# Kernel optimization log

Measured on AMD Instinct MI355X. Metric: run time of the kernel, lower is better.

Reference implementation:

```python
import jax, jax.numpy as jnp
import numpy as np

# Model hyperparameters (from init_kwargs)
B, C, H, W = 4, 3, 224, 224
P = 16            # patch size
E = 768           # embed_dim
NH = 12           # num_heads
DH = E // NH      # head dim
L = 2             # num_layers
DFF = 4 * E
OUT = 1000
NP_ = (H // P) * (W // P)   # 196 patches
ALPHA, BETA, GAMMA = 0.5, 0.5, 1.0
EPS = 1e-8
LN_EPS = 1e-5


def _layernorm(x, w, b):
    mu = x.mean(-1, keepdims=True)
    var = ((x - mu) ** 2).mean(-1, keepdims=True)
    return (x - mu) * jax.lax.rsqrt(var + LN_EPS) * w + b


def _tversky_attn(x, ln_w, ln_b, w_qkv, b_qkv, w_o, b_o):
    # x: [B,S,E]
    h = _layernorm(x, ln_w, ln_b)
    qkv = h @ w_qkv + b_qkv                       # [B,S,3E]
    q, k, v = jnp.split(qkv, 3, axis=-1)
    def heads(t):
        return t.reshape(t.shape[0], t.shape[1], NH, DH).transpose(0, 2, 1, 3)  # [B,NH,S,DH]
    q, k, v = heads(q), heads(k), heads(v)
    # Tversky similarity on non-negative feature memberships
    qp = jax.nn.relu(q)
    kp = jax.nn.relu(k)
    qs = qp.sum(-1)                               # [B,NH,S]
    ks = kp.sum(-1)                               # [B,NH,S]
    # pairwise L1: sum_d |q_i - k_j|   (dominant intermediate [B,NH,S,S,DH])
    l1 = jnp.abs(qp[:, :, :, None, :] - kp[:, :, None, :, :]).sum(-1)  # [B,NH,S,S]
    qsum = qs[:, :, :, None]
    ksum = ks[:, :, None, :]
    inter = 0.5 * (qsum + ksum - l1)              # sum min(q,k)
    a_minus_b = 0.5 * (l1 + qsum - ksum)          # sum relu(q-k)
    b_minus_a = 0.5 * (l1 - qsum + ksum)          # sum relu(k-q)
    scores = GAMMA * inter / (inter + ALPHA * a_minus_b + BETA * b_minus_a + EPS)
    attn = jax.nn.softmax(scores, axis=-1)        # [B,NH,S,S]
    o = jnp.einsum('bhij,bhjd->bhid', attn, v)    # [B,NH,S,DH]
    o = o.transpose(0, 2, 1, 3).reshape(x.shape[0], x.shape[1], E)
    return o @ w_o + b_o


def _forward(x, conv_w, conv_b, pos_embed, cls_token,
             ln1_w, ln1_b, attn_w, attn_b, proj_w, proj_b,
             ln2_w, ln2_b, fc1_w, fc1_b, fc2_w, fc2_b,
             lnf_w, lnf_b, head_w, head_b):
    b = x.shape[0]
    # patch embed: stride==kernel conv == non-overlapping patch projection
    xp = x.reshape(b, C, H // P, P, W // P, P)
    tok = jnp.einsum('bchpwq,ecpq->bhwe', xp, conv_w).reshape(b, NP_, E) + conv_b
    tok = tok + pos_embed                         # [B,196,E]
    cls = jnp.broadcast_to(cls_token, (b, 1, E))
    h = jnp.concatenate([cls, tok], axis=1)       # [B,197,E]
    for i in range(L):
        h = h + _tversky_attn(h, ln1_w[i], ln1_b[i], attn_w[i], attn_b[i], proj_w[i], proj_b[i])
        m = _layernorm(h, ln2_w[i], ln2_b[i])
        m = jax.nn.gelu(m @ fc1_w[i] + fc1_b[i])
        h = h + m @ fc2_w[i] + fc2_b[i]
    h = _layernorm(h, lnf_w, lnf_b)
    return h[:, 0] @ head_w + head_b              # [B,OUT]


def setup_inputs() -> dict:
    key = jax.random.key(0)
    ks = jax.random.split(key, 24)
    n = lambda k, shp, s=0.02: jax.random.normal(k, shp, dtype=jnp.float32) * s
    return {
        'x': jax.random.normal(ks[0], (B, C, H, W), dtype=jnp.float32),
        'conv_w': n(ks[1], (E, C, P, P)),
        'conv_b': jnp.zeros((E,), jnp.float32),
        'pos_embed': n(ks[2], (1, NP_, E)),
        'cls_token': n(ks[3], (1, 1, E)),
        'ln1_w': jnp.ones((L, E), jnp.float32),
        'ln1_b': jnp.zeros((L, E), jnp.float32),
        'attn_w': n(ks[4], (L, E, 3 * E)),
        'attn_b': jnp.zeros((L, 3 * E), jnp.float32),
        'proj_w': n(ks[5], (L, E, E)),
        'proj_b': jnp.zeros((L, E), jnp.float32),
        'ln2_w': jnp.ones((L, E), jnp.float32),
        'ln2_b': jnp.zeros((L, E), jnp.float32),
        'fc1_w': n(ks[6], (L, E, DFF)),
        'fc1_b': jnp.zeros((L, DFF), jnp.float32),
        'fc2_w': n(ks[7], (L, DFF, E)),
        'fc2_b': jnp.zeros((L, E), jnp.float32),
        'lnf_w': jnp.ones((E,), jnp.float32),
        'lnf_b': jnp.zeros((E,), jnp.float32),
        'head_w': n(ks[8], (E, OUT)),
        'head_b': jnp.zeros((OUT,), jnp.float32),
    }


def reference(x, conv_w, conv_b, pos_embed, cls_token,
              ln1_w, ln1_b, attn_w, attn_b, proj_w, proj_b,
              ln2_w, ln2_b, fc1_w, fc1_b, fc2_w, fc2_b,
              lnf_w, lnf_b, head_w, head_b):
    return _forward(x, conv_w, conv_b, pos_embed, cls_token,
                    ln1_w, ln1_b, attn_w, attn_b, proj_w, proj_b,
                    ln2_w, ln2_b, fc1_w, fc1_b, fc2_w, fc2_b,
                    lnf_w, lnf_b, head_w, head_b)
```

## Files before the change

### kernel.cpp

```cpp
#include <hip/hip_runtime.h>
#include <hip/hip_bf16.h>
#include <math.h>

#define B_  4
#define E_  768
#define NH_ 12
#define DH_ 64
#define DFF_ 3072
#define OUT_ 1000
#define S_  197
#define ROWS_ 788
#define QH_P 12608
#define KGP  16384

typedef __bf16 bf16x8_t __attribute__((ext_vector_type(8)));
typedef float f32x4_t __attribute__((ext_vector_type(4)));
typedef _Float16 f16x2_t __attribute__((ext_vector_type(2)));

#define HAS_FDOT2 __has_builtin(__builtin_amdgcn_fdot2)

__device__ __forceinline__ float gelu_f(float x) {
    float x3 = x * x * x;
    return 0.5f * x * (1.0f + tanhf(0.7978845608028654f * (x + 0.044715f * x3)));
}
__device__ __forceinline__ ushort f_to_bf16bits(float f) {
    __hip_bfloat16 b = __float2bfloat16(f);
    return *(ushort*)&b;
}
__device__ __forceinline__ ushort f_to_f16bits(float f) {
    _Float16 h = (_Float16)f;
    return __builtin_bit_cast(ushort, h);
}
__device__ __forceinline__ f16x2_t u2h(uint u) { return __builtin_bit_cast(f16x2_t, u); }
__device__ __forceinline__ f16x2_t min2(f16x2_t a, f16x2_t b) {
    return __builtin_elementwise_min(a, b);
}

#define WT_CONV   0
#define WT_LBASE  589824
#define WT_LSTRIDE 7077888
#define WT_QKV    0
#define WT_PROJ   1769472
#define WT_FC1    2359296
#define WT_FC2    4718592
__global__ __launch_bounds__(256) void prep_all_kernel(const float* __restrict__ x,
                                                       __hip_bfloat16* __restrict__ aim,
                                                       const float* __restrict__ attn_w,
                                                       const float* __restrict__ proj_w,
                                                       const float* __restrict__ fc1_w,
                                                       const float* __restrict__ fc2_w,
                                                       const float* __restrict__ conv_w,
                                                       __hip_bfloat16* __restrict__ wt,
                                                       ushort* __restrict__ vgt) {
    int bid = blockIdx.x;
    if (bid < 588) {
        int id = bid * 256 + threadIdx.x;
        int row = id / 192, k4 = (id - row * 192) * 4;
        int b = row / 196, pr = row - b * 196;
        int hp = pr / 14, wp = pr - hp * 14;
        int c = k4 >> 8, rem = k4 & 255, p = rem >> 4, q = rem & 15;
        float4 v = *(const float4*)&x[(((size_t)(b * 3 + c) * 224) + hp * 16 + p) * 224 + wp * 16 + q];
        ushort4 o = make_ushort4(f_to_bf16bits(v.x), f_to_bf16bits(v.y), f_to_bf16bits(v.z), f_to_bf16bits(v.w));
        *(ushort4*)((ushort*)aim + (size_t)row * 768 + k4) = o;
        return;
    }
    int id = bid - 588;
    if (id < 3456) {
        int l = id / 1728, r = id - l * 1728;
        const float* src;
        __hip_bfloat16* dst;
        int K, N, tile;
        size_t lbase = WT_LBASE + (size_t)l * WT_LSTRIDE;
        if (r < 432)       { src = attn_w + (size_t)l * E_ * 3 * E_; dst = wt + lbase + WT_QKV;  K = E_;   N = 3 * E_; tile = r; }
        else if (r < 576)  { src = proj_w + (size_t)l * E_ * E_;     dst = wt + lbase + WT_PROJ; K = E_;   N = E_;     tile = r - 432; }
        else if (r < 1152) { src = fc1_w + (size_t)l * E_ * DFF_;    dst = wt + lbase + WT_FC1;  K = E_;   N = DFF_;   tile = r - 576; }
        else               { src = fc2_w + (size_t)l * DFF_ * E_;    dst = wt + lbase + WT_FC2;  K = DFF_; N = E_;     tile = r - 1152; }
        int ntn = N >> 6;
        int kb = (tile / ntn) * 64, nb = (tile % ntn) * 64;
        int kq = (threadIdx.x & 15) * 4, nq = (threadIdx.x >> 4) * 4;
        const float* s0 = src + (size_t)(kb + kq) * N + nb + nq;
        float4 v0 = *(const float4*)(s0);
        float4 v1 = *(const float4*)(s0 + N);
        float4 v2 = *(const float4*)(s0 + 2 * N);
        float4 v3 = *(const float4*)(s0 + 3 * N);
        __hip_bfloat16* d0 = dst + (size_t)(nb + nq) * K + kb + kq;
        *(ushort4*)(d0)         = make_ushort4(f_to_bf16bits(v0.x), f_to_bf16bits(v1.x), f_to_bf16bits(v2.x), f_to_bf16bits(v3.x));
        *(ushort4*)(d0 + K)     = make_ushort4(f_to_bf16bits(v0.y), f_to_bf16bits(v1.y), f_to_bf16bits(v2.y), f_to_bf16bits(v3.y));
        *(ushort4*)(d0 + 2 * K) = make_ushort4(f_to_bf16bits(v0.z), f_to_bf16bits(v1.z), f_to_bf16bits(v2.z), f_to_bf16bits(v3.z));
        *(ushort4*)(d0 + 3 * K) = make_ushort4(f_to_bf16bits(v0.w), f_to_bf16bits(v1.w), f_to_bf16bits(v2.w), f_to_bf16bits(v3.w));
        return;
    }
    id -= 3456;
    if (id < 576) {
        int off = (id * 256 + threadIdx.x) * 4;
        float4 v = *(const float4*)&conv_w[off];
        ushort4 o = make_ushort4(f_to_bf16bits(v.x), f_to_bf16bits(v.y), f_to_bf16bits(v.z), f_to_bf16bits(v.w));
        *(ushort4*)((ushort*)wt + WT_CONV + off) = o;
        return;
    }
    id -= 576;
    {
        int off = (id * 256 + threadIdx.x) * 4;
        *(ushort4*)&vgt[off] = make_ushort4(0, 0, 0, 0);
    }
}

#define BK 64
#define AP 72
__global__ __launch_bounds__(256) void gemm_mfma_kernel(const __hip_bfloat16* __restrict__ A,
                                                        const __hip_bfloat16* __restrict__ WT,
                                                        const float* __restrict__ bias,
                                                        const float* __restrict__ res,
                                                        float* __restrict__ Cf,
                                                        __hip_bfloat16* __restrict__ Cb,
                                                        float* __restrict__ partbase,
                                                        int M, int N, int K, int act, int KS,
                                                        int res_pitch, int pn, int nofs) {
    __shared__ __align__(16) ushort Asb[2][64 * AP];
    __shared__ __align__(16) ushort Bsb[2][64 * AP];
    const int tid = threadIdx.x;
    const int wave = tid >> 6, lane = tid & 63;
    const int quad = lane >> 4, l15 = lane & 15;
    const int wm = wave >> 1, wn = wave & 1;
    const int m0 = blockIdx.y * 64, n0 = blockIdx.x * 64;

    const int Kc   = K / KS;
    const int kbeg = blockIdx.z * Kc;
    const int n_it = Kc / BK;

    f32x4_t acc[2][2] = {};

    const int c0r = tid >> 3,         c0o = (tid & 7) * 8;
    const int c1r = (tid + 256) >> 3, c1o = c0o;

    uint4 pa0, pa1, pb0, pb1;
    auto load_tile = [&](int kk) {
        pa0 = make_uint4(0, 0, 0, 0);
        pa1 = pa0;
        int gm = m0 + c0r;
        if (gm < M) pa0 = *(const uint4*)&A[(size_t)gm * K + kk + c0o];
        gm = m0 + c1r;
        if (gm < M) pa1 = *(const uint4*)&A[(size_t)gm * K + kk + c1o];
        pb0 = *(const uint4*)&WT[(size_t)(n0 + c0r) * K + kk + c0o];
        pb1 = *(const uint4*)&WT[(size_t)(n0 + c1r) * K + kk + c1o];
    };
    auto store_tile = [&](int buf) {
        *(uint4*)&Asb[buf][c0r * AP + c0o] = pa0;
        *(uint4*)&Asb[buf][c1r * AP + c1o] = pa1;
        *(uint4*)&Bsb[buf][c0r * AP + c0o] = pb0;
        *(uint4*)&Bsb[buf][c1r * AP + c1o] = pb1;
    };

    load_tile(kbeg);
    store_tile(0);
    if (n_it > 1) load_tile(kbeg + BK);
    __syncthreads();

    for (int it = 0; it < n_it; ++it) {
        const int cur = it & 1, nxt = cur ^ 1;
        if (it + 1 < n_it) {
            store_tile(nxt);
            if (it + 2 < n_it) load_tile(kbeg + (it + 2) * BK);
        }
        const ushort* As = Asb[cur];
        const ushort* Bs = Bsb[cur];
#pragma unroll
        for (int ks = 0; ks < BK; ks += 32) {
            bf16x8_t a0 = *(const bf16x8_t*)&As[(32 * wm + l15) * AP + ks + 8 * quad];
            bf16x8_t a1 = *(const bf16x8_t*)&As[(32 * wm + 16 + l15) * AP + ks + 8 * quad];
            bf16x8_t b0 = *(const bf16x8_t*)&Bs[(32 * wn + l15) * AP + ks + 8 * quad];
            bf16x8_t b1 = *(const bf16x8_t*)&Bs[(32 * wn + 16 + l15) * AP + ks + 8 * quad];
            acc[0][0] = __builtin_amdgcn_mfma_f32_16x16x32_bf16(a0, b0, acc[0][0], 0, 0, 0);
            acc[0][1] = __builtin_amdgcn_mfma_f32_16x16x32_bf16(a0, b1, acc[0][1], 0, 0, 0);
            acc[1][0] = __builtin_amdgcn_mfma_f32_16x16x32_bf16(a1, b0, acc[1][0], 0, 0, 0);
            acc[1][1] = __builtin_amdgcn_mfma_f32_16x16x32_bf16(a1, b1, acc[1][1], 0, 0, 0);
        }
        __syncthreads();
    }

    if (partbase) {
        float* P = partbase + (size_t)blockIdx.z * M * pn;
#pragma unroll
        for (int mi = 0; mi < 2; ++mi)
#pragma unroll
            for (int ni = 0; ni < 2; ++ni) {
                int gn = n0 + 32 * wn + 16 * ni + l15;
#pragma unroll
                for (int r = 0; r < 4; ++r) {
                    int gm = m0 + 32 * wm + 16 * mi + quad * 4 + r;
                    if (gm < M) P[(size_t)gm * pn + nofs + gn] = acc[mi][ni][r];
                }
            }
        return;
    }

#pragma unroll
    for (int mi = 0; mi < 2; ++mi)
#pragma unroll
        for (int ni = 0; ni < 2; ++ni) {
            int gn = n0 + 32 * wn + 16 * ni + l15;
#pragma unroll
            for (int r = 0; r < 4; ++r) {
                int gm = m0 + 32 * wm + 16 * mi + quad * 4 + r;
                if (gm < M) {
                    float v = acc[mi][ni][r] + bias[gn];
                    if (act == 1) v = gelu_f(v);
                    if (res) v += res[(size_t)gm * res_pitch + gn];
                    if (Cf) Cf[(size_t)gm * N + gn] = v;
                    else    Cb[(size_t)gm * N + gn] = __float2bfloat16(v);
                }
            }
        }
}

__global__ __launch_bounds__(256) void gemm_qkv_kernel(const __hip_bfloat16* __restrict__ A,
                                                       const __hip_bfloat16* __restrict__ WT,
                                                       const float* __restrict__ ab,
                                                       ushort* __restrict__ qg,
                                                       float* __restrict__ qsg,
                                                       ushort* __restrict__ kg,
                                                       float* __restrict__ ksg,
                                                       ushort* __restrict__ vgt,
                                                       int ncol0, int nqkv,
                                                       const float* __restrict__ wraw) {
    const int tid = threadIdx.x;
    const int wave = tid >> 6, lane = tid & 63;

    if ((int)blockIdx.x >= nqkv) {
        if (blockIdx.y >= NH_) return;
        const int hh = blockIdx.y, bb = blockIdx.x - nqkv;
        const int head = bb * NH_ + hh;
        __shared__ float sacc[4][64];
        const __hip_bfloat16* xr = A + (size_t)(bb * S_) * E_;
        const float* wcol = wraw + hh * DH_;
        float acc = 0.f;
        const int k0 = wave * 192;
#pragma unroll 4
        for (int k = k0; k < k0 + 192; ++k)
            acc += __bfloat162float(xr[k]) * wcol[(size_t)k * (3 * E_) + lane];
        sacc[wave][lane] = acc;
        __syncthreads();
        if (tid < 64) {
            float q = sacc[0][tid] + sacc[1][tid] + sacc[2][tid] + sacc[3][tid] + ab[hh * DH_ + tid];
            q = fmaxf(q, 0.f);
            qg[(size_t)head * QH_P + tid] = f_to_f16bits(q);
            float s = q;
#pragma unroll
            for (int m = 1; m < 64; m <<= 1) s += __shfl_xor(s, m, 64);
            if (tid == 0) qsg[(size_t)head * 200] = s;
        }
        return;
    }

    __shared__ __align__(16) ushort Asb[2][64 * AP];
    __shared__ __align__(16) ushort Bsb[2][64 * AP];
    __shared__ float rs[2][64];
    const int quad = lane >> 4, l15 = lane & 15;
    const int wm = wave >> 1, wn = wave & 1;
    const int m0 = blockIdx.y * 64;
    const int n0g = ncol0 + blockIdx.x * 64;

    f32x4_t acc[2][2] = {};

    const int c0r = tid >> 3,         c0o = (tid & 7) * 8;
    const int c1r = (tid + 256) >> 3, c1o = c0o;

    uint4 pa0, pa1, pb0, pb1;
    auto load_tile = [&](int kk) {
        pa0 = make_uint4(0, 0, 0, 0);
        pa1 = pa0;
        int gm = m0 + c0r;
        if (gm < ROWS_) pa0 = *(const uint4*)&A[(size_t)gm * E_ + kk + c0o];
        gm = m0 + c1r;
        if (gm < ROWS_) pa1 = *(const uint4*)&A[(size_t)gm * E_ + kk + c1o];
        pb0 = *(const uint4*)&WT[(size_t)(n0g + c0r) * E_ + kk + c0o];
        pb1 = *(const uint4*)&WT[(size_t)(n0g + c1r) * E_ + kk + c1o];
    };
    auto store_tile = [&](int buf) {
        *(uint4*)&Asb[buf][c0r * AP + c0o] = pa0;
        *(uint4*)&Asb[buf][c1r * AP + c1o] = pa1;
        *(uint4*)&Bsb[buf][c0r * AP + c0o] = pb0;
        *(uint4*)&Bsb[buf][c1r * AP + c1o] = pb1;
    };

    load_tile(0);
    store_tile(0);
    load_tile(BK);
    __syncthreads();

    const int n_it = E_ / BK;
    for (int it = 0; it < n_it; ++it) {
        const int cur = it & 1, nxt = cur ^ 1;
        if (it + 1 < n_it) {
            store_tile(nxt);
            if (it + 2 < n_it) load_tile((it + 2) * BK);
        }
        const ushort* As = Asb[cur];
        const ushort* Bs = Bsb[cur];
#pragma unroll
        for (int ks = 0; ks < BK; ks += 32) {
            bf16x8_t a0 = *(const bf16x8_t*)&As[(32 * wm + l15) * AP + ks + 8 * quad];
            bf16x8_t a1 = *(const bf16x8_t*)&As[(32 * wm + 16 + l15) * AP + ks + 8 * quad];
            bf16x8_t b0 = *(const bf16x8_t*)&Bs[(32 * wn + l15) * AP + ks + 8 * quad];
            bf16x8_t b1 = *(const bf16x8_t*)&Bs[(32 * wn + 16 + l15) * AP + ks + 8 * quad];
            acc[0][0] = __builtin_amdgcn_mfma_f32_16x16x32_bf16(a0, b0, acc[0][0], 0, 0, 0);
            acc[0][1] = __builtin_amdgcn_mfma_f32_16x16x32_bf16(a0, b1, acc[0][1], 0, 0, 0);
            acc[1][0] = __builtin_amdgcn_mfma_f32_16x16x32_bf16(a1, b0, acc[1][0], 0, 0, 0);
            acc[1][1] = __builtin_amdgcn_mfma_f32_16x16x32_bf16(a1, b1, acc[1][1], 0, 0, 0);
        }
        __syncthreads();
    }

    const int region = n0g / 768;
    const int hh = (n0g >> 6) % 12;
    const float bias0 = ab[n0g + 32 * wn + l15];
    const float bias1 = ab[n0g + 32 * wn + 16 + l15];

    float rsum[2][4] = {};
#pragma unroll
    for (int mi = 0; mi < 2; ++mi)
#pragma unroll
        for (int ni = 0; ni < 2; ++ni) {
            const int d = 32 * wn + 16 * ni + l15;
#pragma unroll
            for (int r = 0; r < 4; ++r) {
                int gm = m0 + 32 * wm + 16 * mi + quad * 4 + r;
                if (gm < ROWS_) {
                    float v = acc[mi][ni][r] + (ni ? bias1 : bias0);
                    int b = gm / S_, j = gm - b * S_;
                    int head = b * NH_ + hh;
                    if (region == 0) {
                        v = fmaxf(v, 0.f);
                        qg[(size_t)head * QH_P + j * 64 + d] = f_to_f16bits(v);
                        rsum[mi][r] += v;
                    } else if (region == 1) {
                        v = fmaxf(v, 0.f);
                        kg[(size_t)head * KGP + j * 64 + d] = f_to_f16bits(v);
                        rsum[mi][r] += v;
                    } else {
                        vgt[(size_t)head * KGP + d * 256 + j] = f_to_bf16bits(v);
                    }
                }
            }
        }

    if (region < 2) {
#pragma unroll
        for (int mi = 0; mi < 2; ++mi)
#pragma unroll
            for (int r = 0; r < 4; ++r) {
                float s = rsum[mi][r];
                s += __shfl_xor(s, 1, 64);
                s += __shfl_xor(s, 2, 64);
                s += __shfl_xor(s, 4, 64);
                s += __shfl_xor(s, 8, 64);
                rsum[mi][r] = s;
            }
        if (l15 == 0) {
#pragma unroll
            for (int mi = 0; mi < 2; ++mi)
#pragma unroll
                for (int r = 0; r < 4; ++r)
                    rs[wn][32 * wm + 16 * mi + quad * 4 + r] = rsum[mi][r];
        }
        __syncthreads();
        if (tid < 64) {
            int gm = m0 + tid;
            if (gm < ROWS_) {
                int b = gm / S_, j = gm - b * S_;
                int head = b * NH_ + hh;
                float s = rs[0][tid] + rs[1][tid];
                if (region == 0) qsg[(size_t)head * 200 + j] = s;
                else             ksg[(size_t)head * 256 + j] = s;
            }
        }
    }
}

__global__ __launch_bounds__(256) void embed_ln_kernel(const float* __restrict__ p0,
                                                       const float* __restrict__ p1,
                                                       const float* __restrict__ cb,
                                                       const float* __restrict__ pe,
                                                       const float* __restrict__ ct,
                                                       const float* __restrict__ lw,
                                                       const float* __restrict__ lb,
                                                       float* __restrict__ h,
                                                       __hip_bfloat16* __restrict__ y) {
    int row = blockIdx.x, tid = threadIdx.x;
    int b = row / S_, s = row - b * S_;
    float v[3];
#pragma unroll
    for (int c = 0; c < 3; ++c) {
        int e = tid + c * 256;
        float t;
        if (s == 0) t = ct[e];
        else {
            int pr = s - 1;
            size_t gi = (size_t)(b * 196 + pr) * E_ + e;
            t = p0[gi] + p1[gi] + cb[e] + pe[(size_t)pr * E_ + e];
        }
        h[(size_t)row * E_ + e] = t;
        v[c] = t;
    }
    float sm = v[0] + v[1] + v[2];
    float sq = v[0] * v[0] + v[1] * v[1] + v[2] * v[2];
#pragma unroll
    for (int m = 1; m < 64; m <<= 1) {
        sm += __shfl_xor(sm, m, 64);
        sq += __shfl_xor(sq, m, 64);
    }
    __shared__ float ss[4], sqs[4];
    int wave = tid >> 6, lane = tid & 63;
    if (lane == 0) { ss[wave] = sm; sqs[wave] = sq; }
    __syncthreads();
    sm = ss[0] + ss[1] + ss[2] + ss[3];
    sq = sqs[0] + sqs[1] + sqs[2] + sqs[3];
    float mu   = sm * (1.0f / 768.0f);
    float var  = sq * (1.0f / 768.0f) - mu * mu;
    float rstd = rsqrtf(var + 1e-5f);
    __hip_bfloat16* yr = y + (size_t)row * E_;
#pragma unroll
    for (int c = 0; c < 3; ++c) {
        int e = tid + c * 256;
        yr[e] = __float2bfloat16((v[c] - mu) * rstd * lw[e] + lb[e]);
    }
}

__global__ __launch_bounds__(256) void layernorm_kernel(const float* __restrict__ x,
                                                        const float* __restrict__ w,
                                                        const float* __restrict__ b,
                                                        __hip_bfloat16* __restrict__ y) {
    int row = blockIdx.x;
    const float* xr = x + (size_t)row * E_;
    int tid = threadIdx.x;
    float v0 = xr[tid], v1 = xr[tid + 256], v2 = xr[tid + 512];
    float s  = v0 + v1 + v2;
    float sq = v0 * v0 + v1 * v1 + v2 * v2;
#pragma unroll
    for (int m = 1; m < 64; m <<= 1) {
        s  += __shfl_xor(s, m, 64);
        sq += __shfl_xor(sq, m, 64);
    }
    __shared__ float ss[4], sqs[4];
    int wave = tid >> 6, lane = tid & 63;
    if (lane == 0) { ss[wave] = s; sqs[wave] = sq; }
    __syncthreads();
    s  = ss[0] + ss[1] + ss[2] + ss[3];
    sq = sqs[0] + sqs[1] + sqs[2] + sqs[3];
    float mu   = s * (1.0f / 768.0f);
    float var  = sq * (1.0f / 768.0f) - mu * mu;
    float rstd = rsqrtf(var + 1e-5f);
    __hip_bfloat16* yr = y + (size_t)row * E_;
    yr[tid]       = __float2bfloat16((v0 - mu) * rstd * w[tid]       + b[tid]);
    yr[tid + 256] = __float2bfloat16((v1 - mu) * rstd * w[tid + 256] + b[tid + 256]);
    yr[tid + 512] = __float2bfloat16((v2 - mu) * rstd * w[tid + 512] + b[tid + 512]);
}

__global__ __launch_bounds__(256) void reduce_ln_kernel(const float* __restrict__ parts,
                                                        int np, size_t pstride,
                                                        const float* __restrict__ bias,
                                                        float* __restrict__ h,
                                                        const float* __restrict__ lw,
                                                        const float* __restrict__ lb,
                                                        __hip_bfloat16* __restrict__ y) {
    int row = blockIdx.x, tid = threadIdx.x;
    float v[3];
#pragma unroll
    for (int c = 0; c < 3; ++c) {
        int e = tid + c * 256;
        size_t gi = (size_t)row * E_ + e;
        float t = bias[e] + h[gi];
        for (int z = 0; z < np; ++z) t += parts[z * pstride + gi];
        h[gi] = t;
        v[c] = t;
    }
    float s  = v[0] + v[1] + v[2];
    float sq = v[0] * v[0] + v[1] * v[1] + v[2] * v[2];
#pragma unroll
    for (int m = 1; m < 64; m <<= 1) {
        s  += __shfl_xor(s, m, 64);
        sq += __shfl_xor(sq, m, 64);
    }
    __shared__ float ss[4], sqs[4];
    int wave = tid >> 6, lane = tid & 63;
    if (lane == 0) { ss[wave] = s; sqs[wave] = sq; }
    __syncthreads();
    s  = ss[0] + ss[1] + ss[2] + ss[3];
    sq = sqs[0] + sqs[1] + sqs[2] + sqs[3];
    float mu   = s * (1.0f / 768.0f);
    float var  = sq * (1.0f / 768.0f) - mu * mu;
    float rstd = rsqrtf(var + 1e-5f);
    __hip_bfloat16* yr = y + (size_t)row * E_;
#pragma unroll
    for (int c = 0; c < 3; ++c) {
        int e = tid + c * 256;
        yr[e] = __float2bfloat16((v[c] - mu) * rstd * lw[e] + lb[e]);
    }
}

__global__ __launch_bounds__(256) void tversky_attn_kernel(const ushort* __restrict__ qg,
                                                           const ushort* __restrict__ kg,
                                                           const float* __restrict__ ksg,
                                                           const ushort* __restrict__ vgt,
                                                           const float* __restrict__ qsg,
                                                           __hip_bfloat16* __restrict__ ao,
                                                           int nrows) {
    __shared__ __align__(16) ushort kf[16384];
    __shared__ __align__(16) float ks_l[256];
    __shared__ __align__(16) ushort q_l[1024];
    __shared__ __align__(16) ushort p_l[4096];
    __shared__ __align__(16) float den_l[16];

    const int tid = threadIdx.x, wv = tid >> 6, lane = tid & 63;
    const int quad = lane >> 4, l15 = lane & 15;
    const int ch = blockIdx.x, hh = blockIdx.y, bb = blockIdx.z;
    const int head = bb * NH_ + hh;

    {
        const ushort* kgh = kg + (size_t)head * KGP;
#pragma unroll
        for (int g = 0; g < 8; ++g) {
            int idx = g * 256 + tid;
            int row = idx >> 3, c = idx & 7;
            int sw = c ^ ((row >> 1) & 7);
            uint4 kv;
            if (row < S_) kv = *(const uint4*)&kgh[idx * 8];
            else kv = make_uint4(0xD400D400u, 0xD400D400u, 0xD400D400u, 0xD400D400u);
            *(uint4*)&kf[row * 64 + sw * 8] = kv;
        }
        ks_l[tid] = (tid < S_) ? ksg[(size_t)head * 256 + tid] : 0.f;
    }
    const int i0 = ch * 16 + wv * 4;
    if (lane < 32) {
        int r = lane >> 3, c = lane & 7;
        int i = i0 + r;
        uint4 qv = make_uint4(0, 0, 0, 0);
        if (i < nrows) qv = *(const uint4*)&qg[(size_t)head * QH_P + i * 64 + c * 8];
        *(uint4*)&q_l[wv * 256 + r * 64 + c * 8] = qv;
    }
    float qs_r[4];
#pragma unroll
    for (int r = 0; r < 4; ++r)
        qs_r[r] = (i0 + r < nrows) ? qsg[(size_t)head * 200 + i0 + r] : 0.f;
    __syncthreads();

#if HAS_FDOT2
    const f16x2_t one2 = __builtin_bit_cast(f16x2_t, 0x3C003C00u);
#endif
    float den_r[4] = {0.f, 0.f, 0.f, 0.f};
#pragma unroll
    for (int ph = 0; ph < 2; ++ph) {
        const int jb = ph * 128;
        const int r0 = (jb + 2 * lane) * 64;
        float acc0[4] = {0.f, 0.f, 0.f, 0.f};
        float acc1[4] = {0.f, 0.f, 0.f, 0.f};
#pragma unroll 1
        for (int hf = 0; hf < 2; ++hf) {
            uint4 kreg0[4], kreg1[4];
#pragma unroll
            for (int c = 0; c < 4; ++c) {
                int sw = ((hf * 4 + c) ^ (lane & 7)) * 8;
                kreg0[c] = *(const uint4*)&kf[r0 + sw];
                kreg1[c] = *(const uint4*)&kf[r0 + 64 + sw];
            }
#pragma unroll
            for (int c = 0; c < 4; ++c) {
                int cc = hf * 4 + c;
                uint k0p[4] = {kreg0[c].x, kreg0[c].y, kreg0[c].z, kreg0[c].w};
                uint k1p[4] = {kreg1[c].x, kreg1[c].y, kreg1[c].z, kreg1[c].w};
#pragma unroll
                for (int r = 0; r < 4; ++r) {
                    uint4 qu = *(const uint4*)&q_l[wv * 256 + r * 64 + cc * 8];
                    uint qp[4] = {qu.x, qu.y, qu.z, qu.w};
#if HAS_FDOT2
#pragma unroll
                    for (int p = 0; p < 4; ++p) {
                        f16x2_t qq = u2h(qp[p]);
                        acc0[r] = __builtin_amdgcn_fdot2(min2(qq, u2h(k0p[p])), one2, acc0[r], false);
                        acc1[r] = __builtin_amdgcn_fdot2(min2(qq, u2h(k1p[p])), one2, acc1[r], false);
                    }
#else
                    f16x2_t m0 = min2(u2h(qp[0]), u2h(k0p[0]));
                    f16x2_t m1 = min2(u2h(qp[0]), u2h(k1p[0]));
#pragma unroll
                    for (int p = 1; p < 4; ++p) {
                        m0 = m0 + min2(u2h(qp[p]), u2h(k0p[p]));
                        m1 = m1 + min2(u2h(qp[p]), u2h(k1p[p]));
                    }
                    acc0[r] += (float)m0[0] + (float)m0[1];
                    acc1[r] += (float)m1[0] + (float)m1[1];
#endif
                }
            }
        }
        float2 ks2 = *(const float2*)&ks_l[jb + 2 * lane];
#pragma unroll
        for (int r = 0; r < 4; ++r) {
            float s0 = qs_r[r] + ks2.x, s1 = qs_r[r] + ks2.y;
            float e0 = __expf((2.f * acc0[r]) / (s0 + 2e-8f));
            float e1 = __expf((2.f * acc1[r]) / (s1 + 2e-8f));
            float sum = e0 + e1;
#pragma unroll
            for (int m = 1; m < 64; m <<= 1) sum += __shfl_xor(sum, m, 64);
            den_r[r] += sum;
            uint pw = (uint)f_to_bf16bits(e0) | ((uint)f_to_bf16bits(e1) << 16);
            int i = wv * 4 + r;
            *(uint*)&p_l[(i * 256 + jb + 2 * lane) ^ ((i & 7) * 8)] = pw;
        }
    }
    if (lane == 0) {
#pragma unroll
        for (int r = 0; r < 4; ++r) den_l[wv * 4 + r] = den_r[r];
    }
    __syncthreads();

    const ushort* vb = vgt + (size_t)head * KGP + (size_t)(16 * wv + l15) * 256;
    f32x4_t accv = {0.f, 0.f, 0.f, 0.f};
#pragma unroll
    for (int st = 0; st < 8; ++st) {
        bf16x8_t a = *(const bf16x8_t*)&p_l[(l15 * 256 + st * 32 + quad * 8) ^ ((l15 & 7) * 8)];
        bf16x8_t b = *(const bf16x8_t*)&vb[st * 32 + quad * 8];
        accv = __builtin_amdgcn_mfma_f32_16x16x32_bf16(a, b, accv, 0, 0, 0);
    }
    float4 dv = *(const float4*)&den_l[quad * 4];
    float dar[4] = {dv.x, dv.y, dv.z, dv.w};
#pragma unroll
    for (int t = 0; t < 4; ++t) {
        int ig = ch * 16 + quad * 4 + t;
        if (ig < nrows)
            ao[((size_t)(bb * nrows + ig)) * E_ + hh * DH_ + 16 * wv + l15] =
                __float2bfloat16(accv[t] / dar[t]);
    }
}

__global__ __launch_bounds__(256) void head_ln_kernel(const float* __restrict__ hc,
                                                      const float* __restrict__ pc0,
                                                      const float* __restrict__ pc1,
                                                      const float* __restrict__ fb,
                                                      const float* __restrict__ lw,
                                                      const float* __restrict__ lb,
                                                      const float* __restrict__ hw,
                                                      const float* __restrict__ hb,
                                                      float* __restrict__ out) {
    int b = blockIdx.y;
    int tid = threadIdx.x;
    const float* xr0 = hc  + (size_t)b * E_;
    const float* pr0 = pc0 + (size_t)b * E_;
    const float* pr1 = pc1 + (size_t)b * E_;
    float v0 = xr0[tid]       + pr0[tid]       + pr1[tid]       + fb[tid];
    float v1 = xr0[tid + 256] + pr0[tid + 256] + pr1[tid + 256] + fb[tid + 256];
    float v2 = xr0[tid + 512] + pr0[tid + 512] + pr1[tid + 512] + fb[tid + 512];
    float s  = v0 + v1 + v2;
    float sq = v0 * v0 + v1 * v1 + v2 * v2;
#pragma unroll
    for (int m = 1; m < 64; m <<= 1) {
        s  += __shfl_xor(s, m, 64);
        sq += __shfl_xor(sq, m, 64);
    }
    __shared__ float ss[4], sqs[4];
    __shared__ float xr[E_];
    __shared__ float partial[4][64];
    int wave = tid >> 6, lane = tid & 63;
    if (lane == 0) { ss[wave] = s; sqs[wave] = sq; }
    __syncthreads();
    s  = ss[0] + ss[1] + ss[2] + ss[3];
    sq = sqs[0] + sqs[1] + sqs[2] + sqs[3];
    float mu   = s * (1.0f / 768.0f);
    float var  = sq * (1.0f / 768.0f) - mu * mu;
    float rstd = rsqrtf(var + 1e-5f);
    xr[tid]       = (v0 - mu) * rstd * lw[tid]       + lb[tid];
    xr[tid + 256] = (v1 - mu) * rstd * lw[tid + 256] + lb[tid + 256];
    xr[tid + 512] = (v2 - mu) * rstd * lw[tid + 512] + lb[tid + 512];
    __syncthreads();
    int nl = tid & 63, eq = tid >> 6;
    int n = blockIdx.x * 64 + nl;
    float acc = 0.f;
    if (n < OUT_) {
        int e0 = eq * 192;
        for (int e = e0; e < e0 + 192; ++e) acc += xr[e] * hw[(size_t)e * OUT_ + n];
    }
    partial[eq][nl] = acc;
    __syncthreads();
    if (eq == 0 && n < OUT_)
        out[(size_t)b * OUT_ + n] = partial[0][nl] + partial[1][nl] + partial[2][nl] + partial[3][nl] + hb[n];
}

extern "C" void kernel_launch(void* const* d_in, const int* in_sizes, int n_in,
                              void* d_out, int out_size, void* d_ws, size_t ws_size,
                              hipStream_t stream) {
    const float* x        = (const float*)d_in[0];
    const float* conv_w   = (const float*)d_in[1];
    const float* conv_b   = (const float*)d_in[2];
    const float* pos_e    = (const float*)d_in[3];
    const float* cls_t    = (const float*)d_in[4];
    const float* ln1_w    = (const float*)d_in[5];
    const float* ln1_b    = (const float*)d_in[6];
    const float* attn_w   = (const float*)d_in[7];
    const float* attn_b   = (const float*)d_in[8];
    const float* proj_w   = (const float*)d_in[9];
    const float* proj_b   = (const float*)d_in[10];
    const float* ln2_w    = (const float*)d_in[11];
    const float* ln2_b    = (const float*)d_in[12];
    const float* fc1_w    = (const float*)d_in[13];
    const float* fc1_b    = (const float*)d_in[14];
    const float* fc2_w    = (const float*)d_in[15];
    const float* fc2_b    = (const float*)d_in[16];
    const float* lnf_w    = (const float*)d_in[17];
    const float* lnf_b    = (const float*)d_in[18];
    const float* head_w   = (const float*)d_in[19];
    const float* head_b   = (const float*)d_in[20];
    float* out = (float*)d_out;

    float* h       = (float*)d_ws;
    float* part0q  = h + 605184;
    float* part1q  = part0q + 1815552;
    float* part    = part1q + 1815552;
    float* hc      = part + 3631104;
    float* partc   = hc + 3072;
    float* ksg     = partc + 6144;
    float* qsg     = ksg + 12288;
    __hip_bfloat16* lnb  = (__hip_bfloat16*)(qsg + 9600);
    __hip_bfloat16* ao   = lnb + 605184;
    __hip_bfloat16* hid  = ao + 605184;
    __hip_bfloat16* aim  = hid + 2420736;
    __hip_bfloat16* wt   = aim + 602112;
    ushort* kg  = (ushort*)(wt + 14745600);
    ushort* vgt = kg + 786432;
    ushort* qg  = vgt + 786432;
    __hip_bfloat16* lnb4 = (__hip_bfloat16*)(qg + 605184);
    __hip_bfloat16* hid4 = lnb4 + 3072;

    prep_all_kernel<<<5388, 256, 0, stream>>>(x, aim, attn_w, proj_w, fc1_w, fc2_w, conv_w, wt, vgt);
    {
        dim3 grid(E_ / 64, 13, 2);
        gemm_mfma_kernel<<<grid, 256, 0, stream>>>(aim, wt + WT_CONV, nullptr, nullptr, nullptr,
                                                   nullptr, part, 784, E_, E_, 0, 2, 0, E_, 0);
    }
    embed_ln_kernel<<<ROWS_, 256, 0, stream>>>(part, part + 602112, conv_b,
                                               pos_e, cls_t, ln1_w, ln1_b, h, lnb);

    {
        const __hip_bfloat16* wl = wt + WT_LBASE;
        {
            dim3 grid(36, 13);
            gemm_qkv_kernel<<<grid, 256, 0, stream>>>(lnb, wl + WT_QKV, attn_b,
                                                      qg, qsg, kg, ksg, vgt, 0, 36, nullptr);
        }
        tversky_attn_kernel<<<dim3(13, NH_, B_), 256, 0, stream>>>(
            qg, kg, ksg, vgt, qsg, ao, S_);
        {
            dim3 grid(E_ / 64, 13, 2);
            gemm_mfma_kernel<<<grid, 256, 0, stream>>>(ao, wl + WT_PROJ, nullptr, nullptr, nullptr,
                                                       nullptr, part, ROWS_, E_, E_, 0, 2, 0, E_, 0);
        }
        reduce_ln_kernel<<<ROWS_, 256, 0, stream>>>(part, 2, 605184, proj_b,
                                                    h, ln2_w, ln2_b, lnb);
        {
            dim3 grid(DFF_ / 64, 13);
            gemm_mfma_kernel<<<grid, 256, 0, stream>>>(lnb, wl + WT_FC1, fc1_b,
                                                       nullptr, nullptr, hid, nullptr,
                                                       ROWS_, DFF_, E_, 1, 1, 0, DFF_, 0);
        }
        {
            dim3 grid(E_ / 64, 13, 2);
            gemm_mfma_kernel<<<grid, 256, 0, stream>>>(hid, wl + WT_FC2, nullptr, nullptr, nullptr,
                                                       nullptr, part, ROWS_, E_, DFF_, 0, 2, 0, E_, 0);
        }
        reduce_ln_kernel<<<ROWS_, 256, 0, stream>>>(part, 2, 605184, fc2_b,
                                                    h, ln1_w + E_, ln1_b + E_, lnb);
    }

    {
        const __hip_bfloat16* wl = wt + WT_LBASE + WT_LSTRIDE;
        {
            dim3 grid(28, 13);
            gemm_qkv_kernel<<<grid, 256, 0, stream>>>(lnb, wl + WT_QKV, attn_b + 3 * E_,
                                                      qg, qsg, kg, ksg, vgt, 768, 24,
                                                      attn_w + (size_t)E_ * 3 * E_);
        }
        tversky_attn_kernel<<<dim3(1, NH_, B_), 256, 0, stream>>>(
            qg, kg, ksg, vgt, qsg, ao, 1);
        {
            dim3 grid(E_ / 64, 1, 1);
            gemm_mfma_kernel<<<grid, 256, 0, stream>>>(ao, wl + WT_PROJ, proj_b + E_, h,
                                                       hc, nullptr, nullptr,
                                                       4, E_, E_, 0, 1, S_ * E_, E_, 0);
        }
        layernorm_kernel<<<4, 256, 0, stream>>>(hc, ln2_w + E_, ln2_b + E_, lnb4);
        {
            dim3 grid(DFF_ / 64, 1, 1);
            gemm_mfma_kernel<<<grid, 256, 0, stream>>>(lnb4, wl + WT_FC1, fc1_b + DFF_,
                                                       nullptr, nullptr, hid4, nullptr,
                                                       4, DFF_, E_, 1, 1, 0, DFF_, 0);
        }
        {
            dim3 grid(E_ / 64, 1, 2);
            gemm_mfma_kernel<<<grid, 256, 0, stream>>>(hid4, wl + WT_FC2, nullptr, nullptr, nullptr,
                                                       nullptr, partc, 4, E_, DFF_, 0, 2, 0, E_, 0);
        }
    }

    {
        dim3 grid((OUT_ + 63) / 64, B_);
        head_ln_kernel<<<grid, 256, 0, stream>>>(hc, partc, partc + 3072, fc2_b + E_,
                                                 lnf_w, lnf_b, head_w, head_b, out);
    }
}
```

Before: 305.3 us.

## Fuse last-layer CLS tail into one cooperative kernel with grid syncs

Replaces the six small kernels that handle the last layer's CLS-only path (attention, projection, LN2, FC1, FC2, final LN plus head) with one cooperative kernel of 128 blocks that uses grid.sync between stages. The aim is to remove per-launch overhead and the idle gaps between tiny kernels that run on very few rows. The M=4 matmuls now use wave-per-output-column GEMV loops with scalar bf16 loads and shuffle reductions instead of MFMA, and the FC2 split-K partial buffer becomes a single full result. A fallback to the old kernel sequence runs if the cooperative launch fails. The costs are grid-wide barrier latency, and the GEMV loads may be poorly coalesced, since each lane reads scalar bf16 values rather than wide vectors.

```diff
diff --git a/kernel.cpp b/kernel.cpp
--- a/kernel.cpp
+++ b/kernel.cpp
@@ -1,6 +1,9 @@
 #include <hip/hip_runtime.h>
 #include <hip/hip_bf16.h>
+#include <hip/hip_cooperative_groups.h>
 #include <math.h>
+
+namespace cg = cooperative_groups;
 
 #define B_  4
 #define E_  768
@@ -498,13 +501,13 @@
     }
 }
 
-__global__ __launch_bounds__(256) void tversky_attn_kernel(const ushort* __restrict__ qg,
-                                                           const ushort* __restrict__ kg,
-                                                           const float* __restrict__ ksg,
-                                                           const ushort* __restrict__ vgt,
-                                                           const float* __restrict__ qsg,
-                                                           __hip_bfloat16* __restrict__ ao,
-                                                           int nrows) {
+__device__ void tversky_body(const ushort* __restrict__ qg,
+                             const ushort* __restrict__ kg,
+                             const float* __restrict__ ksg,
+                             const ushort* __restrict__ vgt,
+                             const float* __restrict__ qsg,
+                             __hip_bfloat16* __restrict__ ao,
+                             int nrows, int ch, int hh, int bb) {
     __shared__ __align__(16) ushort kf[16384];
     __shared__ __align__(16) float ks_l[256];
     __shared__ __align__(16) ushort q_l[1024];
@@ -513,7 +516,6 @@
 
     const int tid = threadIdx.x, wv = tid >> 6, lane = tid & 63;
     const int quad = lane >> 4, l15 = lane & 15;
-    const int ch = blockIdx.x, hh = blockIdx.y, bb = blockIdx.z;
     const int head = bb * NH_ + hh;
 
     {
@@ -630,6 +632,185 @@
         if (ig < nrows)
             ao[((size_t)(bb * nrows + ig)) * E_ + hh * DH_ + 16 * wv + l15] =
                 __float2bfloat16(accv[t] / dar[t]);
+    }
+}
+
+__global__ __launch_bounds__(256) void tversky_attn_kernel(const ushort* __restrict__ qg,
+                                                           const ushort* __restrict__ kg,
+                                                           const float* __restrict__ ksg,
+                                                           const ushort* __restrict__ vgt,
+                                                           const float* __restrict__ qsg,
+                                                           __hip_bfloat16* __restrict__ ao,
+                                                           int nrows) {
+    tversky_body(qg, kg, ksg, vgt, qsg, ao, nrows, blockIdx.x, blockIdx.y, blockIdx.z);
+}
+
+#define TGRID 128
+__global__ __launch_bounds__(256) void tail_kernel(const ushort* __restrict__ qg,
+                                                   const ushort* __restrict__ kg,
+                                                   const float* __restrict__ ksg,
+                                                   const ushort* __restrict__ vgt,
+                                                   const float* __restrict__ qsg,
+                                                   __hip_bfloat16* __restrict__ ao,
+                                                   const __hip_bfloat16* __restrict__ wproj,
+                                                   const float* __restrict__ projb,
+                                                   const float* __restrict__ h,
+                                                   float* __restrict__ hc,
+                                                   const float* __restrict__ lnw,
+                                                   const float* __restrict__ lnbs,
+                                                   __hip_bfloat16* __restrict__ lnb4,
+                                                   const __hip_bfloat16* __restrict__ wfc1,
+                                                   const float* __restrict__ fc1b,
+                                                   __hip_bfloat16* __restrict__ hid4,
+                                                   const __hip_bfloat16* __restrict__ wfc2,
+                                                   float* __restrict__ fc2f,
+                                                   const float* __restrict__ fb,
+                                                   const float* __restrict__ lw,
+                                                   const float* __restrict__ lb,
+                                                   const float* __restrict__ hw,
+                                                   const float* __restrict__ hb,
+                                                   float* __restrict__ out) {
+    cg::grid_group grid = cg::this_grid();
+    const int tid = threadIdx.x, wv = tid >> 6, lane = tid & 63;
+    const int gw = blockIdx.x * 4 + wv;
+    __shared__ float ss[4], sqs[4];
+    __shared__ float xr[E_];
+    __shared__ float partial[4][64];
+
+    if (blockIdx.x < 48)
+        tversky_body(qg, kg, ksg, vgt, qsg, ao, 1, 0, blockIdx.x % NH_, blockIdx.x / NH_);
+    grid.sync();
+
+    for (int n = gw; n < E_; n += 4 * TGRID) {
+        float acc[4] = {0.f, 0.f, 0.f, 0.f};
+        const __hip_bfloat16* wr = wproj + (size_t)n * E_;
+#pragma unroll
+        for (int kk = 0; kk < 12; ++kk) {
+            int k = lane + kk * 64;
+            float wvv = __bfloat162float(wr[k]);
+#pragma unroll
+            for (int b = 0; b < 4; ++b)
+                acc[b] += __bfloat162float(ao[b * E_ + k]) * wvv;
+        }
+#pragma unroll
+        for (int b = 0; b < 4; ++b)
+#pragma unroll
+            for (int m = 1; m < 64; m <<= 1) acc[b] += __shfl_xor(acc[b], m, 64);
+        if (lane == 0) {
+#pragma unroll
+            for (int b = 0; b < 4; ++b)
+                hc[b * E_ + n] = acc[b] + projb[n] + h[(size_t)(b * S_) * E_ + n];
+        }
+    }
+    grid.sync();
+
+    if (blockIdx.x < 4) {
+        int b = blockIdx.x;
+        const float* x0 = hc + (size_t)b * E_;
+        float v0 = x0[tid], v1 = x0[tid + 256], v2 = x0[tid + 512];
+        float s = v0 + v1 + v2;
+        float sq = v0 * v0 + v1 * v1 + v2 * v2;
+#pragma unroll
+        for (int m = 1; m < 64; m <<= 1) {
+            s  += __shfl_xor(s, m, 64);
+            sq += __shfl_xor(sq, m, 64);
+        }
+        if (lane == 0) { ss[wv] = s; sqs[wv] = sq; }
+        __syncthreads();
+        s  = ss[0] + ss[1] + ss[2] + ss[3];
+        sq = sqs[0] + sqs[1] + sqs[2] + sqs[3];
+        float mu = s * (1.0f / 768.0f);
+        float var = sq * (1.0f / 768.0f) - mu * mu;
+        float rstd = rsqrtf(var + 1e-5f);
+        __hip_bfloat16* yr = lnb4 + (size_t)b * E_;
+        yr[tid]       = __float2bfloat16((v0 - mu) * rstd * lnw[tid]       + lnbs[tid]);
+        yr[tid + 256] = __float2bfloat16((v1 - mu) * rstd * lnw[tid + 256] + lnbs[tid + 256]);
+        yr[tid + 512] = __float2bfloat16((v2 - mu) * rstd * lnw[tid + 512] + lnbs[tid + 512]);
+    }
+    grid.sync();
+
+    for (int n = gw; n < DFF_; n += 4 * TGRID) {
+        float acc[4] = {0.f, 0.f, 0.f, 0.f};
+        const __hip_bfloat16* wr = wfc1 + (size_t)n * E_;
+#pragma unroll
+        for (int kk = 0; kk < 12; ++kk) {
+            int k = lane + kk * 64;
+            float wvv = __bfloat162float(wr[k]);
+#pragma unroll
+            for (int b = 0; b < 4; ++b)
+                acc[b] += __bfloat162float(lnb4[b * E_ + k]) * wvv;
+        }
+#pragma unroll
+        for (int b = 0; b < 4; ++b)
+#pragma unroll
+            for (int m = 1; m < 64; m <<= 1) acc[b] += __shfl_xor(acc[b], m, 64);
+        if (lane == 0) {
+#pragma unroll
+            for (int b = 0; b < 4; ++b)
+                hid4[b * DFF_ + n] = __float2bfloat16(gelu_f(acc[b] + fc1b[n]));
+        }
+    }
+    grid.sync();
+
+    for (int n = gw; n < E_; n += 4 * TGRID) {
+        float acc[4] = {0.f, 0.f, 0.f, 0.f};
+        const __hip_bfloat16* wr = wfc2 + (size_t)n * DFF_;
+#pragma unroll 4
+        for (int kk = 0; kk < 48; ++kk) {
+            int k = lane + kk * 64;
+            float wvv = __bfloat162float(wr[k]);
+#pragma unroll
+            for (int b = 0; b < 4; ++b)
+                acc[b] += __bfloat162float(hid4[b * DFF_ + k]) * wvv;
+        }
+#pragma unroll
+        for (int b = 0; b < 4; ++b)
+#pragma unroll
+            for (int m = 1; m < 64; m <<= 1) acc[b] += __shfl_xor(acc[b], m, 64);
+        if (lane == 0) {
+#pragma unroll
+            for (int b = 0; b < 4; ++b)
+                fc2f[b * E_ + n] = acc[b];
+        }
+    }
+    grid.sync();
+
+    if (blockIdx.x < 64) {
+        int b = blockIdx.x >> 4, ntile = blockIdx.x & 15;
+        const float* x0 = hc + (size_t)b * E_;
+        const float* p0 = fc2f + (size_t)b * E_;
+        float v0 = x0[tid]       + p0[tid]       + fb[tid];
+        float v1 = x0[tid + 256] + p0[tid + 256] + fb[tid + 256];
+        float v2 = x0[tid + 512] + p0[tid + 512] + fb[tid + 512];
+        float s = v0 + v1 + v2;
+        float sq = v0 * v0 + v1 * v1 + v2 * v2;
+#pragma unroll
+        for (int m = 1; m < 64; m <<= 1) {
+            s  += __shfl_xor(s, m, 64);
+            sq += __shfl_xor(sq, m, 64);
+        }
+        if (lane == 0) { ss[wv] = s; sqs[wv] = sq; }
+        __syncthreads();
+        s  = ss[0] + ss[1] + ss[2] + ss[3];
+        sq = sqs[0] + sqs[1] + sqs[2] + sqs[3];
+        float mu = s * (1.0f / 768.0f);
+        float var = sq * (1.0f / 768.0f) - mu * mu;
+        float rstd = rsqrtf(var + 1e-5f);
+        xr[tid]       = (v0 - mu) * rstd * lw[tid]       + lb[tid];
+        xr[tid + 256] = (v1 - mu) * rstd * lw[tid + 256] + lb[tid + 256];
+        xr[tid + 512] = (v2 - mu) * rstd * lw[tid + 512] + lb[tid + 512];
+        __syncthreads();
+        int nl = tid & 63, eq = tid >> 6;
+        int n = ntile * 64 + nl;
+        float acc = 0.f;
+        if (n < OUT_) {
+            int e0 = eq * 192;
+            for (int e = e0; e < e0 + 192; ++e) acc += xr[e] * hw[(size_t)e * OUT_ + n];
+        }
+        partial[eq][nl] = acc;
+        __syncthreads();
+        if (eq == 0 && n < OUT_)
+            out[(size_t)b * OUT_ + n] = partial[0][nl] + partial[1][nl] + partial[2][nl] + partial[3][nl] + hb[n];
     }
 }
 
@@ -716,8 +897,8 @@
     float* part1q  = part0q + 1815552;
     float* part    = part1q + 1815552;
     float* hc      = part + 3631104;
-    float* partc   = hc + 3072;
-    float* ksg     = partc + 6144;
+    float* fc2f    = hc + 3072;
+    float* ksg     = fc2f + 6144;
     float* qsg     = ksg + 12288;
     __hip_bfloat16* lnb  = (__hip_bfloat16*)(qsg + 9600);
     __hip_bfloat16* ao   = lnb + 605184;
@@ -778,31 +959,47 @@
                                                       qg, qsg, kg, ksg, vgt, 768, 24,
                                                       attn_w + (size_t)E_ * 3 * E_);
         }
-        tversky_attn_kernel<<<dim3(1, NH_, B_), 256, 0, stream>>>(
-            qg, kg, ksg, vgt, qsg, ao, 1);
-        {
-            dim3 grid(E_ / 64, 1, 1);
-            gemm_mfma_kernel<<<grid, 256, 0, stream>>>(ao, wl + WT_PROJ, proj_b + E_, h,
-                                                       hc, nullptr, nullptr,
-                                                       4, E_, E_, 0, 1, S_ * E_, E_, 0);
-        }
-        layernorm_kernel<<<4, 256, 0, stream>>>(hc, ln2_w + E_, ln2_b + E_, lnb4);
-        {
-            dim3 grid(DFF_ / 64, 1, 1);
-            gemm_mfma_kernel<<<grid, 256, 0, stream>>>(lnb4, wl + WT_FC1, fc1_b + DFF_,
-                                                       nullptr, nullptr, hid4, nullptr,
-                                                       4, DFF_, E_, 1, 1, 0, DFF_, 0);
-        }
-        {
-            dim3 grid(E_ / 64, 1, 2);
-            gemm_mfma_kernel<<<grid, 256, 0, stream>>>(hid4, wl + WT_FC2, nullptr, nullptr, nullptr,
-                                                       nullptr, partc, 4, E_, DFF_, 0, 2, 0, E_, 0);
-        }
-    }
-
-    {
-        dim3 grid((OUT_ + 63) / 64, B_);
-        head_ln_kernel<<<grid, 256, 0, stream>>>(hc, partc, partc + 3072, fc2_b + E_,
-                                                 lnf_w, lnf_b, head_w, head_b, out);
-    }
-}
+        const __hip_bfloat16* wproj = wl + WT_PROJ;
+        const __hip_bfloat16* wfc1  = wl + WT_FC1;
+        const __hip_bfloat16* wfc2  = wl + WT_FC2;
+        const float* projb1 = proj_b + E_;
+        const float* ln2w1  = ln2_w + E_;
+        const float* ln2b1  = ln2_b + E_;
+        const float* fc1b1  = fc1_b + DFF_;
+        const float* fb1    = fc2_b + E_;
+        const ushort* qg_c = qg; const ushort* kg_c = kg; const ushort* vgt_c = vgt;
+        const float* ksg_c = ksg; const float* qsg_c = qsg;
+        void* args[] = { (void*)&qg_c, (void*)&kg_c, (void*)&ksg_c, (void*)&vgt_c, (void*)&qsg_c,
+                         (void*)&ao, (void*)&wproj, (void*)&projb1, (void*)&h, (void*)&hc,
+                         (void*)&ln2w1, (void*)&ln2b1, (void*)&lnb4, (void*)&wfc1, (void*)&fc1b1,
+                         (void*)&hid4, (void*)&wfc2, (void*)&fc2f, (void*)&fb1,
+                         (void*)&lnf_w, (void*)&lnf_b, (void*)&head_w, (void*)&head_b, (void*)&out };
+        hipError_t cerr = hipLaunchCooperativeKernel((void*)tail_kernel, dim3(TGRID), dim3(256),
+                                                     args, 0, stream);
+        if (cerr != hipSuccess) {
+            tversky_attn_kernel<<<dim3(1, NH_, B_), 256, 0, stream>>>(
+                qg, kg, ksg, vgt, qsg, ao, 1);
+            {
+                dim3 grid(E_ / 64, 1, 1);
+                gemm_mfma_kernel<<<grid, 256, 0, stream>>>(ao, wproj, projb1, h,
+                                                           hc, nullptr, nullptr,
+                                                           4, E_, E_, 0, 1, S_ * E_, E_, 0);
+            }
+            layernorm_kernel<<<4, 256, 0, stream>>>(hc, ln2w1, ln2b1, lnb4);
+            {
+                dim3 grid(DFF_ / 64, 1, 1);
+                gemm_mfma_kernel<<<grid, 256, 0, stream>>>(lnb4, wfc1, fc1b1,
+                                                           nullptr, nullptr, hid4, nullptr,
+                                                           4, DFF_, E_, 1, 1, 0, DFF_, 0);
+            }
+            {
+                dim3 grid(E_ / 64, 1, 2);
+                gemm_mfma_kernel<<<grid, 256, 0, stream>>>(hid4, wfc2, nullptr, nullptr, nullptr,
+                                                           nullptr, fc2f, 4, E_, DFF_, 0, 2, 0, E_, 0);
+            }
+            dim3 grid((OUT_ + 63) / 64, B_);
+            head_ln_kernel<<<grid, 256, 0, stream>>>(hc, fc2f, fc2f + 3072, fb1,
+                                                     lnf_w, lnf_b, head_w, head_b, out);
+        }
+    }
+}
```

Measured after the change: 410.7 us. 34.5% more time.
